# Kernel optimization log

Hardware: AMD Instinct MI355X
Metric: run time of the kernel (lower is better)

## Reference

```python
import jax, jax.numpy as jnp
import numpy as np


def _hungarian(a):
    """Jonker-Volgenant / Kuhn-Munkres shortest-augmenting-path LAP solver.
    a: (n, n) float numpy cost matrix. Returns col_ind (int64, len n) such that
    row i is matched to column col_ind[i] (row_ind is implicitly arange(n),
    exactly like scipy.optimize.linear_sum_assignment on a square matrix).
    """
    n = a.shape[0]
    INF = np.inf
    u = np.zeros(n + 1)
    v = np.zeros(n + 1)
    p = np.zeros(n + 1, dtype=np.int64)   # p[j] = row currently matched to column j
    way = np.zeros(n + 1, dtype=np.int64)
    for i in range(1, n + 1):
        p[0] = i
        j0 = 0
        minv = np.full(n + 1, INF)
        used = np.zeros(n + 1, dtype=bool)
        while True:
            used[j0] = True
            i0 = p[j0]
            cur = a[i0 - 1] - u[i0] - v[1:]          # reduced costs of row i0
            free = ~used[1:]
            better = free & (cur < minv[1:])
            minv[1:] = np.where(better, cur, minv[1:])
            way[1:] = np.where(better, j0, way[1:])
            cand = np.where(free, minv[1:], INF)
            j1 = int(np.argmin(cand)) + 1
            delta = cand[j1 - 1]
            u[p[used]] += delta
            v[used] -= delta
            minv[1:] = np.where(free, minv[1:] - delta, minv[1:])
            j0 = j1
            if p[j0] == 0:
                break
        while j0 != 0:                               # augment along alternating path
            j1 = int(way[j0])
            p[j0] = p[j1]
            j0 = j1
    col_ind = np.zeros(n, dtype=np.int64)
    col_ind[p[1:] - 1] = np.arange(n)
    return col_ind


def _matching(input, target):
    sx = jnp.sum(input * input, axis=-1)
    sy = jnp.sum(target * target, axis=-1)
    cost = sx[:, :, None] + sy[:, None, :] - 2.0 * jnp.einsum('bkd,bmd->bkm', input, target)
    cost_np = np.asarray(jax.device_get(cost), dtype=np.float64)
    perms = np.stack([_hungarian(c) for c in cost_np])  # (B, k)
    return jnp.asarray(perms)


def setup_inputs() -> dict:
    key = jax.random.key(0)
    k1, k2 = jax.random.split(key)
    B, K, D = 512, 128, 512
    return {
        "input": jax.random.normal(k1, (B, K, D), dtype=jnp.float32),
        "target": jax.random.normal(k2, (B, K, D), dtype=jnp.float32),
    }


def reference(input, target):
    # Hungarian assignment is computed on detached costs (constant wrt grads).
    perms = _matching(input, target)                       # (B, k)
    matched_target = jnp.take_along_axis(target, perms[:, :, None], axis=1)
    # Per-batch mean over (k, d), then mean over batch == global mean (equal sizes).
    return jnp.mean((input - matched_target) ** 2)
```

## Files before the change

kernel.cpp:

```cpp
#include <hip/hip_runtime.h>
#include <hip/hip_bf16.h>

#define K_PTS 128
#define DIM   512
#define BK    32
#define XS_STRIDE 132

__device__ __forceinline__ int rdlane_i(int v, int lane) {
    return __builtin_amdgcn_readlane(v, lane);
}
__device__ __forceinline__ float rdlane_f(float v, int lane) {
    return __int_as_float(__builtin_amdgcn_readlane(__float_as_int(v), lane));
}
__device__ __forceinline__ void wave_fence() {
    asm volatile("s_waitcnt lgkmcnt(0)" ::: "memory");
}

__global__ __launch_bounds__(256, 2)
void hungarian_mse_kernel(const float* __restrict__ X, const float* __restrict__ Y,
                          float* __restrict__ out, float inv_total) {
    const int b = blockIdx.x;
    const int t = threadIdx.x;

    __shared__ float A[K_PTS * K_PTS];
    __shared__ float sx_sh[K_PTS];
    __shared__ float sy_sh[K_PTS];
    __shared__ float u_sh[K_PTS];
    __shared__ int   rmatch[K_PTS];
    __shared__ int   wl[512];
    __shared__ int   wl_n;

    float* Xs = A;
    float* Ys = A + BK * XS_STRIDE;

    const float* Xg = X + (size_t)b * K_PTS * DIM;
    const float* Yg = Y + (size_t)b * K_PTS * DIM;

    float acc[8][8];
#pragma unroll
    for (int i = 0; i < 8; ++i)
#pragma unroll
        for (int j = 0; j < 8; ++j) acc[i][j] = 0.0f;

    float nrm = 0.0f;
    const int tx = t & 15;
    const int ty = t >> 4;

    for (int k0 = 0; k0 < DIM; k0 += BK) {
        __syncthreads();
#pragma unroll
        for (int i = 0; i < 4; ++i) {
            int idx = t + i * 256;
            int r  = idx >> 3;
            int kq = idx & 7;
            float4 vx = *(const float4*)(Xg + r * DIM + k0 + kq * 4);
            float4 vy = *(const float4*)(Yg + r * DIM + k0 + kq * 4);
            int kb = kq * 4;
            Xs[(kb + 0) * XS_STRIDE + r] = vx.x;
            Xs[(kb + 1) * XS_STRIDE + r] = vx.y;
            Xs[(kb + 2) * XS_STRIDE + r] = vx.z;
            Xs[(kb + 3) * XS_STRIDE + r] = vx.w;
            Ys[(kb + 0) * XS_STRIDE + r] = vy.x;
            Ys[(kb + 1) * XS_STRIDE + r] = vy.y;
            Ys[(kb + 2) * XS_STRIDE + r] = vy.z;
            Ys[(kb + 3) * XS_STRIDE + r] = vy.w;
        }
        __syncthreads();
        for (int kk = 0; kk < BK; ++kk) {
            const float* xrow = Xs + kk * XS_STRIDE;
            const float* yrow = Ys + kk * XS_STRIDE;
            float4 xa = *(const float4*)(xrow + ty * 8);
            float4 xb = *(const float4*)(xrow + ty * 8 + 4);
            float4 ya = *(const float4*)(yrow + tx * 8);
            float4 yb = *(const float4*)(yrow + tx * 8 + 4);
            float av[8] = {xa.x, xa.y, xa.z, xa.w, xb.x, xb.y, xb.z, xb.w};
            float bv[8] = {ya.x, ya.y, ya.z, ya.w, yb.x, yb.y, yb.z, yb.w};
#pragma unroll
            for (int i = 0; i < 8; ++i)
#pragma unroll
                for (int j = 0; j < 8; ++j)
                    acc[i][j] = fmaf(av[i], bv[j], acc[i][j]);
        }
        if (t < 128) {
#pragma unroll
            for (int kk = 0; kk < BK; ++kk) {
                float v = Xs[kk * XS_STRIDE + t];
                nrm = fmaf(v, v, nrm);
            }
        } else {
#pragma unroll
            for (int kk = 0; kk < BK; ++kk) {
                float v = Ys[kk * XS_STRIDE + (t - 128)];
                nrm = fmaf(v, v, nrm);
            }
        }
    }
    if (t < 128) sx_sh[t] = nrm; else sy_sh[t - 128] = nrm;
    if (t < 128) u_sh[t] = 0.0f;
    __syncthreads();
#pragma unroll
    for (int i = 0; i < 8; ++i) {
        int r = ty * 8 + i;
        float sxr = sx_sh[r];
#pragma unroll
        for (int j = 0; j < 8; ++j) {
            int c = tx * 8 + j;
            A[r * K_PTS + c] = sxr + sy_sh[c] - 2.0f * acc[i][j];
        }
    }
    __syncthreads();

    if (t < 64) {
        float v0, v1;
        int p_lo = -1, p_hi = -1;

        rmatch[t] = -1; rmatch[t + 64] = -1;
        wave_fence();
        {
            float m0 = 1e30f, m1 = 1e30f;
            int a0 = 0, a1 = 0;
#pragma unroll 4
            for (int i = 0; i < K_PTS; ++i) {
                float c0 = A[i * K_PTS + t];
                float c1 = A[i * K_PTS + 64 + t];
                if (c0 < m0) { m0 = c0; a0 = i; }
                if (c1 < m1) { m1 = c1; a1 = i; }
            }
            v0 = m0; v1 = m1;
            int w0 = atomicCAS(&rmatch[a0], -1, (int)t);
            if (w0 == -1) p_lo = a0;
            int w1 = atomicCAS(&rmatch[a1], -1, (int)(t + 64));
            if (w1 == -1) p_hi = a1;
        }
        wave_fence();

        if (t == 0) {
            int n = 0;
            for (int i = 0; i < K_PTS; ++i) if (rmatch[i] < 0) wl[n++] = i;
            wl_n = n;
        }
        wave_fence();

        {
            int head = 0, tail = wl_n, steps = 0;
            while (head < tail && steps < 320) {
                ++steps;
                int i = wl[head++];
                float r0 = fmaxf(A[i * K_PTS + t]      - v0, 0.0f);
                float r1 = fmaxf(A[i * K_PTS + 64 + t] - v1, 0.0f);
                unsigned k0 = (__float_as_uint(r0) & 0xFFFFFF80u) | (unsigned)t;
                unsigned k1 = (__float_as_uint(r1) & 0xFFFFFF80u) | (unsigned)(t + 64);
                unsigned best = min(k0, k1), sec = max(k0, k1);
#pragma unroll
                for (int m = 1; m <= 16; m <<= 1) {
                    unsigned ob = (unsigned)__shfl_xor((int)best, m, 64);
                    unsigned os = (unsigned)__shfl_xor((int)sec,  m, 64);
                    unsigned nb = min(best, ob);
                    unsigned ns = min(max(best, ob), min(sec, os));
                    best = nb; sec = ns;
                }
                unsigned bl = (unsigned)rdlane_i((int)best, 0);
                unsigned bh = (unsigned)rdlane_i((int)best, 32);
                unsigned sl = (unsigned)rdlane_i((int)sec, 0);
                unsigned sh = (unsigned)rdlane_i((int)sec, 32);
                unsigned b2 = min(bl, bh);
                unsigned s2 = min(max(bl, bh), min(sl, sh));
                int j1 = (int)(b2 & 127u);
                int j2 = (int)(s2 & 127u);
                float mu = rdlane_f((j1 >= 64) ? r1 : r0, j1 & 63);
                float nu = rdlane_f((j2 >= 64) ? r1 : r0, j2 & 63);
                if (t == 0) u_sh[i] = nu;
                int kO = rdlane_i((j1 >= 64) ? p_hi : p_lo, j1 & 63);
                bool strict = (mu < nu);
                if (strict && t == (j1 & 63)) {
                    float d = nu - mu;
                    if (j1 >= 64) v1 -= d; else v0 -= d;
                }
                int jA = j1;
                if (!strict && kO >= 0) {
                    int k2 = rdlane_i((j2 >= 64) ? p_hi : p_lo, j2 & 63);
                    if (k2 < 0) jA = j2;
                }
                int kOld = rdlane_i((jA >= 64) ? p_hi : p_lo, jA & 63);
                if (t == (jA & 63)) { if (jA >= 64) p_hi = i; else p_lo = i; }
                if (t == 0) {
                    rmatch[i] = jA;
                    if (kOld >= 0) { rmatch[kOld] = -1; wl[tail] = kOld; }
                }
                if (kOld >= 0) ++tail;
                wave_fence();
            }
        }

        if (t == 0) {
            int n = 0;
            for (int i = 0; i < K_PTS; ++i) if (rmatch[i] < 0) wl[n++] = i;
            wl_n = n;
        }
        wave_fence();
        const int nfree = wl_n;

        for (int idx = 0; idx < nfree; ++idx) {
            int row = wl[idx];
            float u_i = u_sh[row];
            float dist0 = fmaxf(A[row * K_PTS + t]      - u_i - v0, 0.0f);
            float dist1 = fmaxf(A[row * K_PTS + 64 + t] - u_i - v1, 0.0f);
            int way0 = 128, way1 = 128;
            bool sc0 = false, sc1 = false;
            int j1 = 0;
            float D = 0.0f;

            while (true) {
                unsigned k0 = sc0 ? 0xFFFFFFFFu
                                  : ((__float_as_uint(dist0) & 0xFFFFFF80u) | (unsigned)t);
                unsigned k1 = sc1 ? 0xFFFFFFFFu
                                  : ((__float_as_uint(dist1) & 0xFFFFFF80u) | (unsigned)(t + 64));
                unsigned k = min(k0, k1);
#pragma unroll
                for (int m = 1; m <= 16; m <<= 1)
                    k = min(k, (unsigned)__shfl_xor((int)k, m, 64));
                unsigned kl = (unsigned)rdlane_i((int)k, 0);
                unsigned kh = (unsigned)rdlane_i((int)k, 32);
                k = min(kl, kh);
                j1 = (int)(k & 127u);
                int lane = j1 & 63;
                bool hi = j1 >= 64;
                D       = rdlane_f(hi ? dist1 : dist0, lane);
                int i1  = rdlane_i(hi ? p_hi : p_lo, lane);
                if (i1 < 0) break;

                if (j1 == t)      sc0 = true;
                if (j1 == t + 64) sc1 = true;

                float ui1 = u_sh[i1];
                float a0 = A[i1 * K_PTS + t];
                float a1 = A[i1 * K_PTS + 64 + t];
                float base = D - ui1;
                if (!sc0) {
                    float c0 = fmaxf((a0 - v0) + base, 0.0f);
                    if (c0 < dist0) { dist0 = c0; way0 = j1; }
                }
                if (!sc1) {
                    float c1 = fmaxf((a1 - v1) + base, 0.0f);
                    if (c1 < dist1) { dist1 = c1; way1 = j1; }
                }
            }

            if (sc0) { float del = D - dist0; v0 -= del; u_sh[p_lo] += del; }
            if (sc1) { float del = D - dist1; v1 -= del; u_sh[p_hi] += del; }
            if (t == 0) u_sh[row] += D;

            int j0 = j1;
            while (true) {
                int lane0 = j0 & 63;
                bool hi0 = j0 >= 64;
                int jp = rdlane_i(hi0 ? way1 : way0, lane0);
                int pv;
                if (jp == 128) pv = row;
                else           pv = rdlane_i((jp >= 64) ? p_hi : p_lo, jp & 63);
                if (!hi0 && j0 == t)      p_lo = pv;
                if ( hi0 && j0 == t + 64) p_hi = pv;
                if (jp == 128) break;
                j0 = jp;
            }
            wave_fence();
        }

        float tsum = A[p_lo * K_PTS + t] + A[p_hi * K_PTS + 64 + t];
#pragma unroll
        for (int m = 1; m <= 32; m <<= 1)
            tsum += __shfl_xor(tsum, m, 64);
        if (t == 0) atomicAdd(out, tsum * inv_total);
    }
}

extern "C" void kernel_launch(void* const* d_in, const int* in_sizes, int n_in,
                              void* d_out, int out_size, void* d_ws, size_t ws_size,
                              hipStream_t stream) {
    const float* X = (const float*)d_in[0];
    const float* Y = (const float*)d_in[1];
    float* out = (float*)d_out;

    const int total = in_sizes[0];
    const int B = total / (K_PTS * DIM);
    const float inv_total = 1.0f / (float)total;

    hipMemsetAsync(out, 0, out_size * sizeof(float), stream);
    hungarian_mse_kernel<<<dim3(B), dim3(256), 0, stream>>>(X, Y, out, inv_total);
}
```

Baseline: 838.4 us.

## Use DPP wave reductions, add reduction-transfer step, raise solver wave priority

Replaces the shfl_xor butterfly min and two-best reductions with DPP row_shr and row_bcast sequences read from lane 63, which avoids LDS-routed shuffles. Adds a JV-style reduction-transfer pass after column reduction that recomputes u and v for the initially matched rows. This should tighten the duals so augmentation and the search for augmenting paths do less work. Also sets s_setprio 3 on the single solver wave so it is scheduled ahead of co-resident blocks' GEMM waves. The extra preprocessing pass costs O(k^2) LDS reads per block.

```diff
diff --git a/kernel.cpp b/kernel.cpp
--- a/kernel.cpp
+++ b/kernel.cpp
@@ -14,6 +14,40 @@
 }
 __device__ __forceinline__ void wave_fence() {
     asm volatile("s_waitcnt lgkmcnt(0)" ::: "memory");
+}
+
+#define DPP_ID 0xFFFFFFFFu
+
+template <int CTRL, int RM>
+__device__ __forceinline__ unsigned dpp_min1(unsigned k) {
+    unsigned o = (unsigned)__builtin_amdgcn_update_dpp((int)DPP_ID, (int)k, CTRL, RM, 0xF, false);
+    return min(k, o);
+}
+__device__ __forceinline__ unsigned wave_min_u32(unsigned k) {
+    k = dpp_min1<0x111, 0xF>(k);
+    k = dpp_min1<0x112, 0xF>(k);
+    k = dpp_min1<0x114, 0xF>(k);
+    k = dpp_min1<0x118, 0xF>(k);
+    k = dpp_min1<0x142, 0xA>(k);
+    k = dpp_min1<0x143, 0xC>(k);
+    return (unsigned)rdlane_i((int)k, 63);
+}
+template <int CTRL, int RM>
+__device__ __forceinline__ void dpp_min2(unsigned& best, unsigned& sec) {
+    unsigned ob = (unsigned)__builtin_amdgcn_update_dpp((int)DPP_ID, (int)best, CTRL, RM, 0xF, false);
+    unsigned os = (unsigned)__builtin_amdgcn_update_dpp((int)DPP_ID, (int)sec,  CTRL, RM, 0xF, false);
+    sec  = min(max(best, ob), min(sec, os));
+    best = min(best, ob);
+}
+__device__ __forceinline__ void wave_min2_u32(unsigned& best, unsigned& sec) {
+    dpp_min2<0x111, 0xF>(best, sec);
+    dpp_min2<0x112, 0xF>(best, sec);
+    dpp_min2<0x114, 0xF>(best, sec);
+    dpp_min2<0x118, 0xF>(best, sec);
+    dpp_min2<0x142, 0xA>(best, sec);
+    dpp_min2<0x143, 0xC>(best, sec);
+    best = (unsigned)rdlane_i((int)best, 63);
+    sec  = (unsigned)rdlane_i((int)sec, 63);
 }
 
 __global__ __launch_bounds__(256, 2)
@@ -111,6 +145,7 @@
     __syncthreads();
 
     if (t < 64) {
+        asm volatile("s_setprio 3");
         float v0, v1;
         int p_lo = -1, p_hi = -1;
 
@@ -132,6 +167,28 @@
             int w1 = atomicCAS(&rmatch[a1], -1, (int)(t + 64));
             if (w1 == -1) p_hi = a1;
         }
+        wave_fence();
+
+        sy_sh[t] = v0; sy_sh[t + 64] = v1;
+        wave_fence();
+#pragma unroll
+        for (int which = 0; which < 2; ++which) {
+            int i  = t + which * 64;
+            int j1 = rmatch[i];
+            float mu = 1e30f;
+            if (j1 >= 0) {
+#pragma unroll 4
+                for (int s = 0; s < K_PTS; ++s) {
+                    int jj = (s + t) & 127;
+                    float rc = A[i * K_PTS + jj] - sy_sh[jj];
+                    if (jj != j1) mu = fminf(mu, rc);
+                }
+            }
+            sx_sh[i] = mu;
+        }
+        wave_fence();
+        if (p_lo >= 0) { float mu = sx_sh[p_lo]; v0 = A[p_lo * K_PTS + t]      - mu; u_sh[p_lo] = mu; }
+        if (p_hi >= 0) { float mu = sx_sh[p_hi]; v1 = A[p_hi * K_PTS + 64 + t] - mu; u_sh[p_hi] = mu; }
         wave_fence();
 
         if (t == 0) {
@@ -151,22 +208,9 @@
                 unsigned k0 = (__float_as_uint(r0) & 0xFFFFFF80u) | (unsigned)t;
                 unsigned k1 = (__float_as_uint(r1) & 0xFFFFFF80u) | (unsigned)(t + 64);
                 unsigned best = min(k0, k1), sec = max(k0, k1);
-#pragma unroll
-                for (int m = 1; m <= 16; m <<= 1) {
-                    unsigned ob = (unsigned)__shfl_xor((int)best, m, 64);
-                    unsigned os = (unsigned)__shfl_xor((int)sec,  m, 64);
-                    unsigned nb = min(best, ob);
-                    unsigned ns = min(max(best, ob), min(sec, os));
-                    best = nb; sec = ns;
-                }
-                unsigned bl = (unsigned)rdlane_i((int)best, 0);
-                unsigned bh = (unsigned)rdlane_i((int)best, 32);
-                unsigned sl = (unsigned)rdlane_i((int)sec, 0);
-                unsigned sh = (unsigned)rdlane_i((int)sec, 32);
-                unsigned b2 = min(bl, bh);
-                unsigned s2 = min(max(bl, bh), min(sl, sh));
-                int j1 = (int)(b2 & 127u);
-                int j2 = (int)(s2 & 127u);
+                wave_min2_u32(best, sec);
+                int j1 = (int)(best & 127u);
+                int j2 = (int)(sec & 127u);
                 float mu = rdlane_f((j1 >= 64) ? r1 : r0, j1 & 63);
                 float nu = rdlane_f((j2 >= 64) ? r1 : r0, j2 & 63);
                 if (t == 0) u_sh[i] = nu;
@@ -215,13 +259,7 @@
                                   : ((__float_as_uint(dist0) & 0xFFFFFF80u) | (unsigned)t);
                 unsigned k1 = sc1 ? 0xFFFFFFFFu
                                   : ((__float_as_uint(dist1) & 0xFFFFFF80u) | (unsigned)(t + 64));
-                unsigned k = min(k0, k1);
-#pragma unroll
-                for (int m = 1; m <= 16; m <<= 1)
-                    k = min(k, (unsigned)__shfl_xor((int)k, m, 64));
-                unsigned kl = (unsigned)rdlane_i((int)k, 0);
-                unsigned kh = (unsigned)rdlane_i((int)k, 32);
-                k = min(kl, kh);
+                unsigned k = wave_min_u32(min(k0, k1));
                 j1 = (int)(k & 127u);
                 int lane = j1 & 63;
                 bool hi = j1 >= 64;
```

Result: faster. 688.0 us (-17.9%).
